# Performance work log

Measured on AMD Instinct MI355X. Metric: run time of the kernel, lower is better.

Reference implementation:

```python
import jax, jax.numpy as jnp
import numpy as np

B, T, C, H = 16, 512, 256, 8
HS_T = C // H   # temporal head size = 32
HS_S = T // H   # spatial head size = 64
EPS = 1e-6


def _ln(x, w, b):
    m = x.mean(-1, keepdims=True)
    v = ((x - m) ** 2).mean(-1, keepdims=True)
    return (x - m) / jnp.sqrt(v + EPS) * w + b


def setup_inputs() -> dict:
    key = jax.random.key(0)
    ks = jax.random.split(key, 16)
    rn = lambda k, s, scale: jax.random.normal(k, s, dtype=jnp.float32) * scale
    inp = {
        "x_T": rn(ks[0], (B, T, C), 1.0),
        "x_S": rn(ks[1], (B, C, T), 1.0),
        # temporal attention: per-head q/k/v projections, stacked [H, hs, C]
        "Wq_t": rn(ks[2], (H, HS_T, C), C ** -0.5),
        "Wk_t": rn(ks[3], (H, HS_T, C), C ** -0.5),
        "Wv_t": rn(ks[4], (H, HS_T, C), C ** -0.5),
        "Wo": rn(ks[5], (C, C), C ** -0.5),
        # spatial attention: per-head q/k over the time axis, stacked [H, hs_s, T]
        "Wq_s": rn(ks[6], (H, HS_S, T), T ** -0.5),
        "Wk_s": rn(ks[7], (H, HS_S, T), T ** -0.5),
        # feed-forward blocks (expansion_factor=4)
        "ff1_w1": rn(ks[8], (4 * C, C), C ** -0.5),
        "ff1_b1": jnp.zeros((4 * C,), jnp.float32),
        "ff1_w2": rn(ks[9], (C, 4 * C), (4 * C) ** -0.5),
        "ff1_b2": jnp.zeros((C,), jnp.float32),
        "ff2_w1": rn(ks[10], (4 * C, C), C ** -0.5),
        "ff2_b1": jnp.zeros((4 * C,), jnp.float32),
        "ff2_w2": rn(ks[11], (C, 4 * C), (4 * C) ** -0.5),
        "ff2_b2": jnp.zeros((C,), jnp.float32),
        # layernorm affine params
        "t_ln1_w": jnp.ones((C,), jnp.float32), "t_ln1_b": jnp.zeros((C,), jnp.float32),
        "t_ln2_w": jnp.ones((C,), jnp.float32), "t_ln2_b": jnp.zeros((C,), jnp.float32),
        "s_ln1_w": jnp.ones((T,), jnp.float32), "s_ln1_b": jnp.zeros((T,), jnp.float32),
        "fus_ln_w": jnp.ones((C,), jnp.float32), "fus_ln_b": jnp.zeros((C,), jnp.float32),
    }
    return inp


def reference(x_T, x_S, Wq_t, Wk_t, Wv_t, Wo, Wq_s, Wk_s,
              ff1_w1, ff1_b1, ff1_w2, ff1_b2, ff2_w1, ff2_b1, ff2_w2, ff2_b2,
              t_ln1_w, t_ln1_b, t_ln2_w, t_ln2_b, s_ln1_w, s_ln1_b,
              fus_ln_w, fus_ln_b):
    # ---- temporal (causal) multi-head attention ----
    h = _ln(x_T, t_ln1_w, t_ln1_b)                         # [B,T,C]
    q = jnp.einsum('btc,hdc->bhtd', h, Wq_t)
    k = jnp.einsum('btc,hdc->bhtd', h, Wk_t)
    v = jnp.einsum('btc,hdc->bhtd', h, Wv_t)
    scores = jnp.einsum('bhtd,bhsd->bhts', q, k) / jnp.sqrt(jnp.float32(HS_T))
    causal = jnp.tril(jnp.ones((T, T), dtype=bool))
    scores = jnp.where(causal, scores, -jnp.inf)
    att = jax.nn.softmax(scores, axis=-1)
    o = jnp.einsum('bhts,bhsd->bhtd', att, v)              # [B,H,T,hs]
    o = o.transpose(0, 2, 1, 3).reshape(B, T, C)           # concat heads
    attn_out = o @ Wo.T
    x = x_T + attn_out
    # FFN 1
    h2 = _ln(x, t_ln2_w, t_ln2_b)
    f = jax.nn.relu(h2 @ ff1_w1.T + ff1_b1) @ ff1_w2.T + ff1_b2
    temporal_out = x + f                                   # [B,T,C]
    # ---- spatial (non-causal) attention over neurons ----
    hs = _ln(x_S, s_ln1_w, s_ln1_b)                        # [B,C,T]
    qs = jnp.einsum('bct,hdt->bhcd', hs, Wq_s)
    ks = jnp.einsum('bct,hdt->bhcd', hs, Wk_s)
    sc = jnp.einsum('bhcd,bhed->bhce', qs, ks) / jnp.sqrt(jnp.float32(HS_S))
    spatial_weights = jax.nn.softmax(sc, axis=-1).mean(axis=1)   # [B,C,C], mean over heads
    # ---- fusion ----
    fused = jnp.einsum('bce,bte->btc', spatial_weights, temporal_out)
    x2 = temporal_out + fused
    h3 = _ln(x2, fus_ln_w, fus_ln_b)
    f2 = jax.nn.relu(h3 @ ff2_w1.T + ff2_b1) @ ff2_w2.T + ff2_b2
    out = x2 + f2
    return out, spatial_weights
```

## Files before the change

kernel.cpp:

```cpp
#include <hip/hip_runtime.h>
#include <hip/hip_bf16.h>

typedef __hip_bfloat16 bf16;
typedef __attribute__((ext_vector_type(8))) short short8;
typedef __attribute__((ext_vector_type(4))) float f32x4;

#define F_BIAS 1
#define F_RELU 2
#define F_RES  4

__device__ __forceinline__ void st_out(float* p, float v){ *p = v; }
__device__ __forceinline__ void st_out(bf16* p, float v){ *p = __float2bfloat16(v); }
__device__ __forceinline__ short f2bs(float f){
  bf16 h = __float2bfloat16(f);
  return *reinterpret_cast<short*>(&h);
}

__device__ __forceinline__ void gl_lds16(const void* g, void* l){
  __builtin_amdgcn_global_load_lds(
      (const __attribute__((address_space(1))) void*)g,
      (__attribute__((address_space(3))) void*)l, 16, 0, 0);
}

struct ProArgs {
  const float* wsrc[10];
  bf16* wdst[10];
  const float *xT, *xS, *tl1w, *tl1b, *sl1w, *sl1b;
  bf16 *hT, *hS;
};

template<int RL>
__device__ __forceinline__ void wave_ln(bf16* __restrict__ dst,
    const float* __restrict__ src, const float* __restrict__ w,
    const float* __restrict__ bvec, int row){
  int lane = threadIdx.x & 63;
  const float* s = src + (size_t)row*RL;
  float4 v0 = *(const float4*)(s + lane*4);
  float4 v1 = {0.f,0.f,0.f,0.f};
  float sum = v0.x+v0.y+v0.z+v0.w;
  float sq  = v0.x*v0.x+v0.y*v0.y+v0.z*v0.z+v0.w*v0.w;
  if (RL == 512){
    v1 = *(const float4*)(s + 256 + lane*4);
    sum += v1.x+v1.y+v1.z+v1.w;
    sq  += v1.x*v1.x+v1.y*v1.y+v1.z*v1.z+v1.w*v1.w;
  }
  #pragma unroll
  for (int off=32; off; off>>=1){
    sum += __shfl_xor(sum, off, 64);
    sq  += __shfl_xor(sq , off, 64);
  }
  const float inv = 1.0f/(float)RL;
  float mean = sum*inv;
  float rstd = rsqrtf(sq*inv - mean*mean + 1e-6f);
  float4 w0 = *(const float4*)(w + lane*4);
  float4 b0 = *(const float4*)(bvec + lane*4);
  bf16* d = dst + (size_t)row*RL;
  short4 o;
  o.x = f2bs((v0.x-mean)*rstd*w0.x + b0.x);
  o.y = f2bs((v0.y-mean)*rstd*w0.y + b0.y);
  o.z = f2bs((v0.z-mean)*rstd*w0.z + b0.z);
  o.w = f2bs((v0.w-mean)*rstd*w0.w + b0.w);
  *(short4*)((short*)d + lane*4) = o;
  if (RL == 512){
    float4 w1 = *(const float4*)(w + 256 + lane*4);
    float4 b1 = *(const float4*)(bvec + 256 + lane*4);
    short4 o1;
    o1.x = f2bs((v1.x-mean)*rstd*w1.x + b1.x);
    o1.y = f2bs((v1.y-mean)*rstd*w1.y + b1.y);
    o1.z = f2bs((v1.z-mean)*rstd*w1.z + b1.z);
    o1.w = f2bs((v1.w-mean)*rstd*w1.w + b1.w);
    *(short4*)((short*)d + 256 + lane*4) = o1;
  }
}

__global__ __launch_bounds__(256) void prologue(ProArgs a){
  int blk = blockIdx.x;
  int wid = threadIdx.x >> 6;
  if (blk < 1792){
    int v = blk*256 + threadIdx.x;
    int e = v*4;
    int seg = (e>=65536)+(e>=131072)+(e>=196608)+(e>=262144)+(e>=524288)
            + (e>=786432)+(e>=1048576)+(e>=1310720)+(e>=1572864);
    const int starts[10] = {0,65536,131072,196608,262144,524288,786432,
                            1048576,1310720,1572864};
    int off = e - starts[seg];
    float4 f = *(const float4*)(a.wsrc[seg] + off);
    short4 o;
    o.x = f2bs(f.x); o.y = f2bs(f.y); o.z = f2bs(f.z); o.w = f2bs(f.w);
    *(short4*)((short*)a.wdst[seg] + off) = o;
  } else if (blk < 1792 + 2048){
    wave_ln<256>(a.hT, a.xT, a.tl1w, a.tl1b, (blk-1792)*4 + wid);
  } else {
    wave_ln<512>(a.hS, a.xS, a.sl1w, a.sl1b, (blk-3840)*4 + wid);
  }
}

template<int BM, int BK>
__device__ __forceinline__ void gemm_body(
    short* __restrict__ AsB, short* __restrict__ BsB,
    const bf16* __restrict__ A, const bf16* __restrict__ B,
    float* __restrict__ outF, bf16* __restrict__ outB,
    const float* __restrict__ bias, const float* __restrict__ resid,
    int K, int lda, int ldb, int ldc, int flags, int m0, int n0){
  int tid = threadIdx.x;
  int w = tid>>6, lane = tid&63, quad = lane>>4, l16 = lane&15;
  constexpr int WM = BM/2;
  constexpr int MF = WM/16;
  constexpr int CPR = BK/8;
  constexpr int CA = BM*CPR/256;
  constexpr int CB = 128*CPR/256;
  int wm = (w>>1)*WM, wn = (w&1)*64;
  f32x4 acc[MF][4];
  #pragma unroll
  for (int r=0;r<MF;r++)
    #pragma unroll
    for (int j=0;j<4;j++)
      acc[r][j] = (f32x4){0.f,0.f,0.f,0.f};

  auto stage = [&](int k0, int half){
    short* as = AsB + half*(BM*BK);
    short* bs = BsB + half*(128*BK);
    #pragma unroll
    for (int c=0;c<CA;c++){
      int ch = tid + c*256;
      int row = ch / CPR, p = ch % CPR;
      gl_lds16(A + (size_t)(m0+row)*lda + k0 + ((p ^ (row&(CPR-1)))*8),
               &as[row*BK + p*8]);
    }
    #pragma unroll
    for (int c=0;c<CB;c++){
      int ch = tid + c*256;
      int row = ch / CPR, p = ch % CPR;
      gl_lds16(B + (size_t)(n0+row)*ldb + k0 + ((p ^ (row&(CPR-1)))*8),
               &bs[row*BK + p*8]);
    }
  };

  stage(0, 0);
  __syncthreads();
  int nk = K / BK;
  for (int t = 0; t < nk; ++t){
    if (t+1 < nk) stage((t+1)*BK, (t+1)&1);
    const short* as = AsB + (t&1)*(BM*BK);
    const short* bs = BsB + (t&1)*(128*BK);
    #pragma unroll
    for (int ks=0; ks<BK/32; ++ks){
      short8 af[MF], bfr[4];
      #pragma unroll
      for (int r=0;r<MF;r++){
        int rr = wm + r*16 + l16;
        af[r] = *(short8*)&as[rr*BK + (((ks*4+quad) ^ (rr&(CPR-1)))*8)];
      }
      #pragma unroll
      for (int j=0;j<4;j++){
        int rr = wn + j*16 + l16;
        bfr[j] = *(short8*)&bs[rr*BK + (((ks*4+quad) ^ (rr&(CPR-1)))*8)];
      }
      #pragma unroll
      for (int r=0;r<MF;r++)
        #pragma unroll
        for (int j=0;j<4;j++)
          acc[r][j] = __builtin_amdgcn_mfma_f32_16x16x32_bf16(af[r], bfr[j], acc[r][j], 0,0,0);
    }
    __syncthreads();
  }
  #pragma unroll
  for (int r=0;r<MF;r++){
    int mb = m0 + wm + r*16 + quad*4;
    #pragma unroll
    for (int j=0;j<4;j++){
      int n = n0 + wn + j*16 + l16;
      float bv = (flags & F_BIAS) ? bias[n] : 0.0f;
      #pragma unroll
      for (int e=0;e<4;e++){
        float v = acc[r][j][e] + bv;
        if (flags & F_RELU) v = fmaxf(v, 0.0f);
        long long idx = (long long)(mb+e)*ldc + n;
        if (flags & F_RES) v += resid[idx];
        if (outF) outF[idx] = v;
        if (outB) st_out(outB + idx, v);
      }
    }
  }
}

template<int BM, int BK>
__global__ __launch_bounds__(256) void gemm_mfma(
    const bf16* __restrict__ A, const bf16* __restrict__ B,
    float* __restrict__ outF, bf16* __restrict__ outB,
    const float* __restrict__ bias, const float* __restrict__ resid,
    int K, int lda, int ldb, int ldc, int flags){
  __shared__ __align__(16) short As[2*BM*BK];
  __shared__ __align__(16) short Bs[2*128*BK];
  gemm_body<BM,BK>(As,Bs,A,B,outF,outB,bias,resid,K,lda,ldb,ldc,flags,
                   blockIdx.x*BM, blockIdx.y*128);
}

struct GArgs {
  const bf16 *A, *B;
  float* outF; bf16* outB;
  const float *bias, *resid;
  int K, lda, ldb, ldc, flags, ty;
};
__global__ __launch_bounds__(256) void gemm_dual(GArgs g0, GArgs g1, int n0){
  __shared__ __align__(16) short As[2*128*64];
  __shared__ __align__(16) short Bs[2*128*64];
  int id = blockIdx.x;
  bool first = id < n0;
  const GArgs& g = first ? g0 : g1;
  int t = first ? id : id - n0;
  int bx = t / g.ty, by = t - bx*g.ty;
  gemm_body<128,64>(As, Bs, g.A, g.B, g.outF, g.outB, g.bias, g.resid,
                    g.K, g.lda, g.ldb, g.ldc, g.flags, bx*128, by*128);
}

__global__ __launch_bounds__(256) void gemm_ln(
    const bf16* __restrict__ A, const bf16* __restrict__ B,
    float* __restrict__ outF, bf16* __restrict__ outLN,
    const float* __restrict__ resid,
    const float* __restrict__ lnw, const float* __restrict__ lnb,
    int K, int lda, int ldb, int flags,
    long long sA, long long sB, long long sO, long long sR){
  int bz = blockIdx.z;
  A += (size_t)bz*sA;
  B += (size_t)bz*sB;
  long long obase = (long long)bz*sO;
  __shared__ __align__(16) short As[2*32*64];
  __shared__ __align__(16) short Bs[2*256*64];
  __shared__ float redS[2][32], redQ[2][32];
  int tid = threadIdx.x;
  int m0 = blockIdx.x*32;
  int w = tid>>6, lane = tid&63, quad = lane>>4, l16 = lane&15;
  int wm = (w>>1)*16, wn = (w&1)*128;
  f32x4 acc[8];
  #pragma unroll
  for (int j=0;j<8;j++) acc[j] = (f32x4){0.f,0.f,0.f,0.f};

  auto stage = [&](int k0, int half){
    short* as = As + half*(32*64);
    short* bs = Bs + half*(256*64);
    {
      int row = tid >> 3, p = tid & 7;
      gl_lds16(A + (size_t)(m0+row)*lda + k0 + ((p ^ (row&7))*8),
               &as[row*64 + p*8]);
    }
    #pragma unroll
    for (int c=0;c<8;c++){
      int ch = tid + c*256;
      int row = ch >> 3, p = ch & 7;
      gl_lds16(B + (size_t)row*ldb + k0 + ((p ^ (row&7))*8),
               &bs[row*64 + p*8]);
    }
  };

  stage(0, 0);
  __syncthreads();
  int nk = K / 64;
  for (int t = 0; t < nk; ++t){
    if (t+1 < nk) stage((t+1)*64, (t+1)&1);
    const short* as = As + (t&1)*(32*64);
    const short* bs = Bs + (t&1)*(256*64);
    #pragma unroll
    for (int ks=0; ks<2; ++ks){
      int rr = wm + l16;
      short8 af = *(short8*)&as[rr*64 + (((ks*4+quad) ^ (rr&7))*8)];
      #pragma unroll
      for (int j=0;j<8;j++){
        int rb = wn + j*16 + l16;
        short8 bfr = *(short8*)&bs[rb*64 + (((ks*4+quad) ^ (rb&7))*8)];
        acc[j] = __builtin_amdgcn_mfma_f32_16x16x32_bf16(af, bfr, acc[j], 0,0,0);
      }
    }
    __syncthreads();
  }
  #pragma unroll
  for (int e=0;e<4;e++){
    int row = wm + quad*4 + e;
    float s = 0.f, q2 = 0.f;
    #pragma unroll
    for (int j=0;j<8;j++){
      float v = acc[j][e];
      if (flags & F_RES)
        v += resid[(long long)bz*sR + (long long)(m0+row)*256 + wn + j*16 + l16];
      acc[j][e] = v;
      s += v; q2 += v*v;
    }
    #pragma unroll
    for (int off=1; off<16; off<<=1){
      s  += __shfl_xor(s , off, 16);
      q2 += __shfl_xor(q2, off, 16);
    }
    if (l16==0){ redS[w&1][row] = s; redQ[w&1][row] = q2; }
  }
  __syncthreads();
  #pragma unroll
  for (int e=0;e<4;e++){
    int row = wm + quad*4 + e;
    float tot = redS[0][row] + redS[1][row];
    float tq  = redQ[0][row] + redQ[1][row];
    float mean = tot * (1.0f/256.0f);
    float var  = tq * (1.0f/256.0f) - mean*mean;
    float rstd = rsqrtf(var + 1e-6f);
    #pragma unroll
    for (int j=0;j<8;j++){
      int col = wn + j*16 + l16;
      float v = acc[j][e];
      long long idx = obase + (long long)(m0+row)*256 + col;
      if (outF) outF[idx] = v;
      outLN[idx] = __float2bfloat16((v-mean)*rstd*lnw[col] + lnb[col]);
    }
  }
}

__device__ __forceinline__ int fsw(int row){ return (row>>1)&3; }
__global__ __launch_bounds__(256) void flash_mfma(
    const bf16* __restrict__ qkv, bf16* __restrict__ o){
  int qt = (int)gridDim.x - 1 - (int)blockIdx.x;
  int h = blockIdx.y, b = blockIdx.z;
  int tid = threadIdx.x;
  int w = tid>>6, lane = tid&63, quad = lane>>4, l16 = lane&15;
  __shared__ __align__(16) bf16 Qs[64*32];
  __shared__ __align__(16) bf16 Ks[2][64*32];
  __shared__ __align__(16) bf16 Vt[2][32*72];
  __shared__ __align__(16) bf16 Ps[64*72];
  const bf16* base = qkv + (size_t)b*512*768;
  int t0 = qt*64;
  int srow = tid>>2, spos = tid&3;
  gl_lds16(base + (size_t)(t0+srow)*768 + h*32 + ((spos ^ fsw(srow))*8),
           &Qs[srow*32 + spos*8]);
  {
    const bf16* rp = base + (size_t)srow*768 + h*32;
    gl_lds16(rp + 256 + ((spos ^ fsw(srow))*8), &Ks[0][srow*32 + spos*8]);
    short8 v = *(const short8*)(rp + 512 + spos*8);
    #pragma unroll
    for (int q=0;q<8;q++){
      short tmp = v[q];
      Vt[0][(spos*8+q)*72 + srow] = *(bf16*)&tmp;
    }
  }
  f32x4 accO[2];
  accO[0] = (f32x4){0.f,0.f,0.f,0.f};
  accO[1] = (f32x4){0.f,0.f,0.f,0.f};
  float m_i[4], l_i[4];
  #pragma unroll
  for (int e=0;e<4;e++){ m_i[e] = -3.0e38f; l_i[e] = 0.0f; }
  const float scale = 0.17677669529663687f;
  __syncthreads();
  int rq = w*16 + l16;
  short8 aq = *(short8*)&Qs[rq*32 + ((quad ^ fsw(rq))*8)];

  for (int kt = 0; kt <= qt; ++kt){
    int cur = kt&1, nxt = cur^1;
    bool pre = (kt < qt);
    short8 vpre;
    if (pre){
      const bf16* rp = base + (size_t)((kt+1)*64 + srow)*768 + h*32;
      gl_lds16(rp + 256 + ((spos ^ fsw(srow))*8), &Ks[nxt][srow*32 + spos*8]);
      vpre = *(const short8*)(rp + 512 + spos*8);
    }
    f32x4 S[4];
    #pragma unroll
    for (int j2=0;j2<4;j2++){
      int rk = j2*16 + l16;
      short8 bk = *(short8*)&Ks[cur][rk*32 + ((quad ^ fsw(rk))*8)];
      S[j2] = __builtin_amdgcn_mfma_f32_16x16x32_bf16(aq, bk,
                (f32x4){0.f,0.f,0.f,0.f}, 0,0,0);
    }
    bool diag = (kt == qt);
    int s0 = kt*64;
    int qrow_base = t0 + w*16 + quad*4;
    #pragma unroll
    for (int e=0;e<4;e++){
      float sv[4];
      #pragma unroll
      for (int j2=0;j2<4;j2++){
        float x = S[j2][e]*scale;
        if (diag && (s0 + j2*16 + l16 > qrow_base + e)) x = -3.0e38f;
        sv[j2] = x;
      }
      float mx = fmaxf(fmaxf(sv[0],sv[1]), fmaxf(sv[2],sv[3]));
      #pragma unroll
      for (int off=1; off<16; off<<=1) mx = fmaxf(mx, __shfl_xor(mx, off, 64));
      float m_new = fmaxf(m_i[e], mx);
      float alpha = __expf(m_i[e]-m_new);
      float rs = 0.0f;
      #pragma unroll
      for (int j2=0;j2<4;j2++){
        float p = __expf(sv[j2]-m_new);
        rs += p;
        Ps[(w*16+quad*4+e)*72 + j2*16 + l16] = __float2bfloat16(p);
      }
      #pragma unroll
      for (int off=1; off<16; off<<=1) rs += __shfl_xor(rs, off, 64);
      l_i[e] = l_i[e]*alpha + rs;
      m_i[e] = m_new;
      accO[0][e] *= alpha;
      accO[1][e] *= alpha;
    }
    asm volatile("s_waitcnt lgkmcnt(0)" ::: "memory");
    __builtin_amdgcn_sched_barrier(0);
    #pragma unroll
    for (int sh=0; sh<2; ++sh){
      short8 ap = *(short8*)&Ps[(w*16+l16)*72 + sh*32 + quad*8];
      #pragma unroll
      for (int dh=0; dh<2; ++dh){
        short8 bv = *(short8*)&Vt[cur][(dh*16+l16)*72 + sh*32 + quad*8];
        accO[dh] = __builtin_amdgcn_mfma_f32_16x16x32_bf16(ap, bv, accO[dh], 0,0,0);
      }
    }
    if (pre){
      #pragma unroll
      for (int q=0;q<8;q++){
        short tmp = vpre[q];
        Vt[nxt][(spos*8+q)*72 + srow] = *(bf16*)&tmp;
      }
    }
    __syncthreads();
  }
  #pragma unroll
  for (int e=0;e<4;e++){
    float inv = 1.0f/l_i[e];
    int t = t0 + w*16 + quad*4 + e;
    bf16* op = o + ((size_t)(b*512+t))*256 + h*32 + l16;
    op[0]  = __float2bfloat16(accO[0][e]*inv);
    op[16] = __float2bfloat16(accO[1][e]*inv);
  }
}

__device__ void spatial_body(bf16* __restrict__ Qall, bf16* __restrict__ KsB,
                             const bf16* __restrict__ qk,
                             float* __restrict__ out1, bf16* __restrict__ swB,
                             int ct, int b){
  int tid = threadIdx.x;
  int w = tid>>6, lane = tid&63, quad = lane>>4, l16 = lane&15;
  __shared__ float redM[4][16], redS2[4][16];
  const bf16* qbase = qk + ((size_t)(b*256 + ct*16))*1024;
  #pragma unroll
  for (int c=0;c<4;c++){
    int ch = tid + c*256;
    int row = ch>>6, p = ch&63;
    gl_lds16(qbase + (size_t)row*1024 + ((p ^ (row&7))*8), &Qall[row*512 + p*8]);
  }
  auto stageK = [&](int h, int half){
    bf16* ks = KsB + half*(256*64);
    #pragma unroll
    for (int c=0;c<8;c++){
      int ch = tid + c*256;
      int e = ch>>3, p = ch&7;
      gl_lds16(qk + ((size_t)(b*256 + e))*1024 + 512 + h*64 + ((p ^ (e&7))*8),
               &ks[e*64 + p*8]);
    }
  };
  stageK(0, 0);
  float fRes[4][4];
  #pragma unroll
  for (int j=0;j<4;j++)
    #pragma unroll
    for (int e=0;e<4;e++) fRes[j][e] = 0.0f;
  __syncthreads();

  for (int h=0; h<8; ++h){
    if (h < 7) stageK(h+1, (h+1)&1);
    const bf16* kcur = KsB + (h&1)*(256*64);
    f32x4 acc[4];
    #pragma unroll
    for (int j=0;j<4;j++) acc[j] = (f32x4){0.f,0.f,0.f,0.f};
    #pragma unroll
    for (int ki=0; ki<2; ++ki){
      int g = h*8 + ki*4 + quad;
      short8 aq = *(short8*)&Qall[l16*512 + ((g ^ (l16&7))*8)];
      #pragma unroll
      for (int j=0;j<4;j++){
        int e = w*64 + j*16 + l16;
        short8 bk = *(short8*)&kcur[e*64 + (((ki*4+quad) ^ (e&7))*8)];
        acc[j] = __builtin_amdgcn_mfma_f32_16x16x32_bf16(aq, bk, acc[j], 0,0,0);
      }
    }
    #pragma unroll
    for (int e=0;e<4;e++){
      float m = -3.0e38f;
      #pragma unroll
      for (int j=0;j<4;j++){
        float s = acc[j][e]*0.125f;
        acc[j][e] = s;
        m = fmaxf(m, s);
      }
      #pragma unroll
      for (int off=1; off<16; off<<=1) m = fmaxf(m, __shfl_xor(m, off, 16));
      if (l16==0) redM[w][quad*4+e] = m;
    }
    __syncthreads();
    #pragma unroll
    for (int e=0;e<4;e++){
      int r = quad*4+e;
      float m = fmaxf(fmaxf(redM[0][r],redM[1][r]), fmaxf(redM[2][r],redM[3][r]));
      float s = 0.0f;
      #pragma unroll
      for (int j=0;j<4;j++){
        float p = __expf(acc[j][e]-m);
        acc[j][e] = p; s += p;
      }
      #pragma unroll
      for (int off=1; off<16; off<<=1) s += __shfl_xor(s, off, 16);
      if (l16==0) redS2[w][r] = s;
    }
    __syncthreads();
    #pragma unroll
    for (int e=0;e<4;e++){
      int r = quad*4+e;
      float tot = redS2[0][r]+redS2[1][r]+redS2[2][r]+redS2[3][r];
      float inv = 0.125f/tot;
      #pragma unroll
      for (int j=0;j<4;j++) fRes[j][e] += acc[j][e]*inv;
    }
  }
  #pragma unroll
  for (int e=0;e<4;e++){
    int c = ct*16 + quad*4 + e;
    size_t rb = ((size_t)b*256 + c)*256;
    #pragma unroll
    for (int j=0;j<4;j++){
      int col = w*64 + j*16 + l16;
      out1[rb+col] = fRes[j][e];
      swB[rb+col]  = __float2bfloat16(fRes[j][e]);
    }
  }
}

__global__ __launch_bounds__(256) void mixed_l2(
    const bf16* __restrict__ gA, const bf16* __restrict__ gB,
    float* __restrict__ gOutF, bf16* __restrict__ gOutB,
    const float* __restrict__ gBias, const float* __restrict__ gResid,
    const bf16* __restrict__ qk, float* __restrict__ out1,
    bf16* __restrict__ swB){
  __shared__ __align__(16) short lds[40960];
  int id = blockIdx.x;
  if (id < 256){
    int bx = id >> 1, by = id & 1;
    gemm_body<64,64>(lds, lds + 2*64*64, gA, gB, gOutF, gOutB, gBias, gResid,
                     1024, 1024, 1024, 256, F_BIAS|F_RES, bx*64, by*128);
  } else {
    int t = id - 256;
    spatial_body((bf16*)lds, (bf16*)(lds + 8192), qk, out1, swB, t & 15, t >> 4);
  }
}

extern "C" void kernel_launch(void* const* d_in, const int* in_sizes, int n_in,
                              void* d_out, int out_size, void* d_ws, size_t ws_size,
                              hipStream_t stream){
  (void)in_sizes; (void)n_in; (void)out_size; (void)ws_size;
  const float* x_T  = (const float*)d_in[0];
  const float* x_S  = (const float*)d_in[1];
  const float* Wq_t = (const float*)d_in[2];
  const float* Wk_t = (const float*)d_in[3];
  const float* Wv_t = (const float*)d_in[4];
  const float* Wo   = (const float*)d_in[5];
  const float* Wq_s = (const float*)d_in[6];
  const float* Wk_s = (const float*)d_in[7];
  const float* f1w1 = (const float*)d_in[8];
  const float* f1b1 = (const float*)d_in[9];
  const float* f1w2 = (const float*)d_in[10];
  const float* f1b2 = (const float*)d_in[11];
  const float* f2w1 = (const float*)d_in[12];
  const float* f2b1 = (const float*)d_in[13];
  const float* f2w2 = (const float*)d_in[14];
  const float* f2b2 = (const float*)d_in[15];
  const float* tl1w = (const float*)d_in[16];
  const float* tl1b = (const float*)d_in[17];
  const float* tl2w = (const float*)d_in[18];
  const float* tl2b = (const float*)d_in[19];
  const float* sl1w = (const float*)d_in[20];
  const float* sl1b = (const float*)d_in[21];
  const float* flw  = (const float*)d_in[22];
  const float* flb  = (const float*)d_in[23];

  float* ws = (float*)d_ws;
  size_t off = 0;
  bf16*  Wqkvb  = (bf16*)(ws + off); off += 768*256/2;
  bf16*  Wob    = (bf16*)(ws + off); off += 256*256/2;
  bf16*  f1w1b  = (bf16*)(ws + off); off += 1024*256/2;
  bf16*  f1w2b  = (bf16*)(ws + off); off += 256*1024/2;
  bf16*  f2w1b  = (bf16*)(ws + off); off += 1024*256/2;
  bf16*  f2w2b  = (bf16*)(ws + off); off += 256*1024/2;
  bf16*  WSb    = (bf16*)(ws + off); off += 1024*512/2;
  bf16*  bufHb  = (bf16*)(ws + off); off += (size_t)8192*256/2;
  bf16*  bufHSb = (bf16*)(ws + off); off += (size_t)4096*512/2;
  bf16*  bufQKVb= (bf16*)(ws + off); off += (size_t)8192*768/2;
  bf16*  bufBigB= (bf16*)(ws + off); off += (size_t)8192*1024/2;
  bf16*  bufOb  = (bf16*)(ws + off); off += (size_t)8192*256/2;
  bf16*  bufTOb = (bf16*)(ws + off); off += (size_t)8192*256/2;
  bf16*  swB    = (bf16*)(ws + off); off += (size_t)16*256*256/2;
  bf16*  qkB    = (bf16*)(ws + off); off += (size_t)4096*1024/2;
  float* bufX   = ws + off; off += (size_t)8192*256;
  float* bufTO  = ws + off; off += (size_t)8192*256;
  float* bufX2  = ws + off; off += (size_t)8192*256;

  float* out0 = (float*)d_out;
  float* out1 = out0 + (size_t)16*512*256;

  ProArgs pa;
  pa.wsrc[0]=Wq_t;  pa.wdst[0]=Wqkvb;
  pa.wsrc[1]=Wk_t;  pa.wdst[1]=Wqkvb+65536;
  pa.wsrc[2]=Wv_t;  pa.wdst[2]=Wqkvb+131072;
  pa.wsrc[3]=Wo;    pa.wdst[3]=Wob;
  pa.wsrc[4]=f1w1;  pa.wdst[4]=f1w1b;
  pa.wsrc[5]=f1w2;  pa.wdst[5]=f1w2b;
  pa.wsrc[6]=f2w1;  pa.wdst[6]=f2w1b;
  pa.wsrc[7]=f2w2;  pa.wdst[7]=f2w2b;
  pa.wsrc[8]=Wq_s;  pa.wdst[8]=WSb;
  pa.wsrc[9]=Wk_s;  pa.wdst[9]=WSb+262144;
  pa.xT=x_T; pa.xS=x_S; pa.tl1w=tl1w; pa.tl1b=tl1b;
  pa.sl1w=sl1w; pa.sl1b=sl1b; pa.hT=bufHb; pa.hS=bufHSb;
  prologue<<<4864,256,0,stream>>>(pa);

  GArgs gq, gs;
  gq.A=bufHb;  gq.B=Wqkvb; gq.outF=nullptr; gq.outB=bufQKVb;
  gq.bias=nullptr; gq.resid=nullptr;
  gq.K=256; gq.lda=256; gq.ldb=256; gq.ldc=768; gq.flags=0; gq.ty=6;
  gs.A=bufHSb; gs.B=WSb;   gs.outF=nullptr; gs.outB=qkB;
  gs.bias=nullptr; gs.resid=nullptr;
  gs.K=512; gs.lda=512; gs.ldb=512; gs.ldc=1024; gs.flags=0; gs.ty=8;
  gemm_dual<<<640,256,0,stream>>>(gq, gs, 384);

  flash_mfma<<<dim3(8,8,16),256,0,stream>>>(bufQKVb, bufOb);
  gemm_ln<<<dim3(256,1,1),256,0,stream>>>(bufOb, Wob, bufX, bufHb,
        x_T, tl2w, tl2b, 256, 256,256, F_RES, 0,0,0,0);
  gemm_mfma<128,64><<<dim3(64,8),256,0,stream>>>(bufHb, f1w1b, nullptr, bufBigB,
        f1b1, nullptr, 256, 256,256,1024, F_BIAS|F_RELU);
  mixed_l2<<<512,256,0,stream>>>(bufBigB, f1w2b, bufTO, bufTOb, f1b2, bufX,
        qkB, out1, swB);
  gemm_ln<<<dim3(16,1,16),256,0,stream>>>(bufTOb, swB, bufX2, bufHb,
        bufTO, flw, flb, 256, 256,256, F_RES,
        131072, 65536, 131072, 131072);
  gemm_mfma<128,64><<<dim3(64,8),256,0,stream>>>(bufHb, f2w1b, nullptr, bufBigB,
        f2b1, nullptr, 256, 256,256,1024, F_BIAS|F_RELU);
  gemm_mfma<64,64><<<dim3(128,2),256,0,stream>>>(bufBigB, f2w2b, out0, nullptr,
        f2b2, bufX2, 1024, 1024,1024,256, F_BIAS|F_RES);
}
```

Before: 303.4 us.

## Shrink GEMM tiles, widen gemm_ln to 512 threads, split spatial K staging

Generalizes gemm_body to separate BM/BN tiles and halves M tiles for the QKV, FFN and second-layer GEMMs, doubling block counts to fill more CUs. gemm_ln now runs with 8 waves, each covering 64 columns. The spatial attention body stages K in half-head chunks to cut LDS use, which lets mixed_l2 use a smaller shared buffer. The loop barriers move to the top of each iteration, dropping one sync per pipeline step, and LDS-only barriers use an lgkmcnt wait. Smaller tiles give more parallelism but less reuse per block and more redundant loads of B.

```diff
diff --git a/kernel.cpp b/kernel.cpp
--- a/kernel.cpp
+++ b/kernel.cpp
@@ -20,6 +20,11 @@
   __builtin_amdgcn_global_load_lds(
       (const __attribute__((address_space(1))) void*)g,
       (__attribute__((address_space(3))) void*)l, 16, 0, 0);
+}
+
+__device__ __forceinline__ void lgkm_barrier(){
+  asm volatile("s_waitcnt lgkmcnt(0)" ::: "memory");
+  __builtin_amdgcn_s_barrier();
 }
 
 struct ProArgs {
@@ -95,7 +100,7 @@
   }
 }
 
-template<int BM, int BK>
+template<int BM, int BN, int BK>
 __device__ __forceinline__ void gemm_body(
     short* __restrict__ AsB, short* __restrict__ BsB,
     const bf16* __restrict__ A, const bf16* __restrict__ B,
@@ -104,22 +109,22 @@
     int K, int lda, int ldb, int ldc, int flags, int m0, int n0){
   int tid = threadIdx.x;
   int w = tid>>6, lane = tid&63, quad = lane>>4, l16 = lane&15;
-  constexpr int WM = BM/2;
-  constexpr int MF = WM/16;
+  constexpr int MF  = BM/32;
+  constexpr int NF  = BN/32;
   constexpr int CPR = BK/8;
-  constexpr int CA = BM*CPR/256;
-  constexpr int CB = 128*CPR/256;
-  int wm = (w>>1)*WM, wn = (w&1)*64;
-  f32x4 acc[MF][4];
+  constexpr int CA  = BM*CPR/256;
+  constexpr int CB  = BN*CPR/256;
+  int wm = (w>>1)*(BM/2), wn = (w&1)*(BN/2);
+  f32x4 acc[MF][NF];
   #pragma unroll
   for (int r=0;r<MF;r++)
     #pragma unroll
-    for (int j=0;j<4;j++)
+    for (int j=0;j<NF;j++)
       acc[r][j] = (f32x4){0.f,0.f,0.f,0.f};
 
   auto stage = [&](int k0, int half){
     short* as = AsB + half*(BM*BK);
-    short* bs = BsB + half*(128*BK);
+    short* bs = BsB + half*(BN*BK);
     #pragma unroll
     for (int c=0;c<CA;c++){
       int ch = tid + c*256;
@@ -137,38 +142,37 @@
   };
 
   stage(0, 0);
-  __syncthreads();
   int nk = K / BK;
   for (int t = 0; t < nk; ++t){
+    __syncthreads();
     if (t+1 < nk) stage((t+1)*BK, (t+1)&1);
     const short* as = AsB + (t&1)*(BM*BK);
-    const short* bs = BsB + (t&1)*(128*BK);
+    const short* bs = BsB + (t&1)*(BN*BK);
     #pragma unroll
     for (int ks=0; ks<BK/32; ++ks){
-      short8 af[MF], bfr[4];
+      short8 af[MF], bfr[NF];
       #pragma unroll
       for (int r=0;r<MF;r++){
         int rr = wm + r*16 + l16;
         af[r] = *(short8*)&as[rr*BK + (((ks*4+quad) ^ (rr&(CPR-1)))*8)];
       }
       #pragma unroll
-      for (int j=0;j<4;j++){
+      for (int j=0;j<NF;j++){
         int rr = wn + j*16 + l16;
         bfr[j] = *(short8*)&bs[rr*BK + (((ks*4+quad) ^ (rr&(CPR-1)))*8)];
       }
       #pragma unroll
       for (int r=0;r<MF;r++)
         #pragma unroll
-        for (int j=0;j<4;j++)
+        for (int j=0;j<NF;j++)
           acc[r][j] = __builtin_amdgcn_mfma_f32_16x16x32_bf16(af[r], bfr[j], acc[r][j], 0,0,0);
     }
-    __syncthreads();
   }
   #pragma unroll
   for (int r=0;r<MF;r++){
     int mb = m0 + wm + r*16 + quad*4;
     #pragma unroll
-    for (int j=0;j<4;j++){
+    for (int j=0;j<NF;j++){
       int n = n0 + wn + j*16 + l16;
       float bv = (flags & F_BIAS) ? bias[n] : 0.0f;
       #pragma unroll
@@ -184,16 +188,16 @@
   }
 }
 
-template<int BM, int BK>
+template<int BM, int BN, int BK>
 __global__ __launch_bounds__(256) void gemm_mfma(
     const bf16* __restrict__ A, const bf16* __restrict__ B,
     float* __restrict__ outF, bf16* __restrict__ outB,
     const float* __restrict__ bias, const float* __restrict__ resid,
     int K, int lda, int ldb, int ldc, int flags){
   __shared__ __align__(16) short As[2*BM*BK];
-  __shared__ __align__(16) short Bs[2*128*BK];
-  gemm_body<BM,BK>(As,Bs,A,B,outF,outB,bias,resid,K,lda,ldb,ldc,flags,
-                   blockIdx.x*BM, blockIdx.y*128);
+  __shared__ __align__(16) short Bs[2*BN*BK];
+  gemm_body<BM,BN,BK>(As,Bs,A,B,outF,outB,bias,resid,K,lda,ldb,ldc,flags,
+                      blockIdx.x*BM, blockIdx.y*BN);
 }
 
 struct GArgs {
@@ -203,18 +207,18 @@
   int K, lda, ldb, ldc, flags, ty;
 };
 __global__ __launch_bounds__(256) void gemm_dual(GArgs g0, GArgs g1, int n0){
-  __shared__ __align__(16) short As[2*128*64];
+  __shared__ __align__(16) short As[2*64*64];
   __shared__ __align__(16) short Bs[2*128*64];
   int id = blockIdx.x;
   bool first = id < n0;
   const GArgs& g = first ? g0 : g1;
   int t = first ? id : id - n0;
   int bx = t / g.ty, by = t - bx*g.ty;
-  gemm_body<128,64>(As, Bs, g.A, g.B, g.outF, g.outB, g.bias, g.resid,
-                    g.K, g.lda, g.ldb, g.ldc, g.flags, bx*128, by*128);
-}
-
-__global__ __launch_bounds__(256) void gemm_ln(
+  gemm_body<64,128,64>(As, Bs, g.A, g.B, g.outF, g.outB, g.bias, g.resid,
+                       g.K, g.lda, g.ldb, g.ldc, g.flags, bx*64, by*128);
+}
+
+__global__ __launch_bounds__(512) void gemm_ln(
     const bf16* __restrict__ A, const bf16* __restrict__ B,
     float* __restrict__ outF, bf16* __restrict__ outLN,
     const float* __restrict__ resid,
@@ -227,26 +231,27 @@
   long long obase = (long long)bz*sO;
   __shared__ __align__(16) short As[2*32*64];
   __shared__ __align__(16) short Bs[2*256*64];
-  __shared__ float redS[2][32], redQ[2][32];
+  __shared__ float redS[4][32], redQ[4][32];
   int tid = threadIdx.x;
   int m0 = blockIdx.x*32;
   int w = tid>>6, lane = tid&63, quad = lane>>4, l16 = lane&15;
-  int wm = (w>>1)*16, wn = (w&1)*128;
-  f32x4 acc[8];
-  #pragma unroll
-  for (int j=0;j<8;j++) acc[j] = (f32x4){0.f,0.f,0.f,0.f};
+  int wm = (w>>2)*16;
+  int wn = (w&3)*64;
+  f32x4 acc[4];
+  #pragma unroll
+  for (int j=0;j<4;j++) acc[j] = (f32x4){0.f,0.f,0.f,0.f};
 
   auto stage = [&](int k0, int half){
     short* as = As + half*(32*64);
     short* bs = Bs + half*(256*64);
-    {
+    if (tid < 256){
       int row = tid >> 3, p = tid & 7;
       gl_lds16(A + (size_t)(m0+row)*lda + k0 + ((p ^ (row&7))*8),
                &as[row*64 + p*8]);
     }
     #pragma unroll
-    for (int c=0;c<8;c++){
-      int ch = tid + c*256;
+    for (int c=0;c<4;c++){
+      int ch = tid + c*512;
       int row = ch >> 3, p = ch & 7;
       gl_lds16(B + (size_t)row*ldb + k0 + ((p ^ (row&7))*8),
                &bs[row*64 + p*8]);
@@ -254,9 +259,9 @@
   };
 
   stage(0, 0);
-  __syncthreads();
   int nk = K / 64;
   for (int t = 0; t < nk; ++t){
+    __syncthreads();
     if (t+1 < nk) stage((t+1)*64, (t+1)&1);
     const short* as = As + (t&1)*(32*64);
     const short* bs = Bs + (t&1)*(256*64);
@@ -265,20 +270,19 @@
       int rr = wm + l16;
       short8 af = *(short8*)&as[rr*64 + (((ks*4+quad) ^ (rr&7))*8)];
       #pragma unroll
-      for (int j=0;j<8;j++){
+      for (int j=0;j<4;j++){
         int rb = wn + j*16 + l16;
         short8 bfr = *(short8*)&bs[rb*64 + (((ks*4+quad) ^ (rb&7))*8)];
         acc[j] = __builtin_amdgcn_mfma_f32_16x16x32_bf16(af, bfr, acc[j], 0,0,0);
       }
     }
-    __syncthreads();
   }
   #pragma unroll
   for (int e=0;e<4;e++){
     int row = wm + quad*4 + e;
     float s = 0.f, q2 = 0.f;
     #pragma unroll
-    for (int j=0;j<8;j++){
+    for (int j=0;j<4;j++){
       float v = acc[j][e];
       if (flags & F_RES)
         v += resid[(long long)bz*sR + (long long)(m0+row)*256 + wn + j*16 + l16];
@@ -290,19 +294,19 @@
       s  += __shfl_xor(s , off, 16);
       q2 += __shfl_xor(q2, off, 16);
     }
-    if (l16==0){ redS[w&1][row] = s; redQ[w&1][row] = q2; }
+    if (l16==0){ redS[w&3][row] = s; redQ[w&3][row] = q2; }
   }
   __syncthreads();
   #pragma unroll
   for (int e=0;e<4;e++){
     int row = wm + quad*4 + e;
-    float tot = redS[0][row] + redS[1][row];
-    float tq  = redQ[0][row] + redQ[1][row];
+    float tot = redS[0][row] + redS[1][row] + redS[2][row] + redS[3][row];
+    float tq  = redQ[0][row] + redQ[1][row] + redQ[2][row] + redQ[3][row];
     float mean = tot * (1.0f/256.0f);
     float var  = tq * (1.0f/256.0f) - mean*mean;
     float rstd = rsqrtf(var + 1e-6f);
     #pragma unroll
-    for (int j=0;j<8;j++){
+    for (int j=0;j<4;j++){
       int col = wn + j*16 + l16;
       float v = acc[j][e];
       long long idx = obase + (long long)(m0+row)*256 + col;
@@ -350,6 +354,7 @@
   short8 aq = *(short8*)&Qs[rq*32 + ((quad ^ fsw(rq))*8)];
 
   for (int kt = 0; kt <= qt; ++kt){
+    if (kt) __syncthreads();
     int cur = kt&1, nxt = cur^1;
     bool pre = (kt < qt);
     short8 vpre;
@@ -415,7 +420,6 @@
         Vt[nxt][(spos*8+q)*72 + srow] = *(bf16*)&tmp;
       }
     }
-    __syncthreads();
   }
   #pragma unroll
   for (int e=0;e<4;e++){
@@ -441,77 +445,84 @@
     int row = ch>>6, p = ch&63;
     gl_lds16(qbase + (size_t)row*1024 + ((p ^ (row&7))*8), &Qall[row*512 + p*8]);
   }
-  auto stageK = [&](int h, int half){
-    bf16* ks = KsB + half*(256*64);
-    #pragma unroll
-    for (int c=0;c<8;c++){
+  auto stageK = [&](int ck, int half){
+    bf16* ks = KsB + half*(128*64);
+    int h = ck>>1, hf = ck&1;
+    #pragma unroll
+    for (int c=0;c<4;c++){
       int ch = tid + c*256;
-      int e = ch>>3, p = ch&7;
-      gl_lds16(qk + ((size_t)(b*256 + e))*1024 + 512 + h*64 + ((p ^ (e&7))*8),
-               &ks[e*64 + p*8]);
+      int el = ch>>3, p = ch&7;
+      int e  = hf*128 + el;
+      gl_lds16(qk + ((size_t)(b*256 + e))*1024 + 512 + h*64 + ((p ^ (el&7))*8),
+               &ks[el*64 + p*8]);
     }
   };
   stageK(0, 0);
   float fRes[4][4];
   #pragma unroll
-  for (int j=0;j<4;j++)
-    #pragma unroll
-    for (int e=0;e<4;e++) fRes[j][e] = 0.0f;
-  __syncthreads();
-
-  for (int h=0; h<8; ++h){
-    if (h < 7) stageK(h+1, (h+1)&1);
-    const bf16* kcur = KsB + (h&1)*(256*64);
-    f32x4 acc[4];
-    #pragma unroll
-    for (int j=0;j<4;j++) acc[j] = (f32x4){0.f,0.f,0.f,0.f};
+  for (int f=0;f<4;f++)
+    #pragma unroll
+    for (int e=0;e<4;e++) fRes[f][e] = 0.0f;
+  f32x4 acc[4];
+
+  for (int ck=0; ck<16; ++ck){
+    int h = ck>>1, hf = ck&1;
+    __syncthreads();
+    if (ck+1 < 16) stageK(ck+1, (ck+1)&1);
+    const bf16* kcur = KsB + (ck&1)*(128*64);
+    if (hf == 0){
+      #pragma unroll
+      for (int f=0;f<4;f++) acc[f] = (f32x4){0.f,0.f,0.f,0.f};
+    }
     #pragma unroll
     for (int ki=0; ki<2; ++ki){
       int g = h*8 + ki*4 + quad;
       short8 aq = *(short8*)&Qall[l16*512 + ((g ^ (l16&7))*8)];
       #pragma unroll
-      for (int j=0;j<4;j++){
-        int e = w*64 + j*16 + l16;
-        short8 bk = *(short8*)&kcur[e*64 + (((ki*4+quad) ^ (e&7))*8)];
-        acc[j] = __builtin_amdgcn_mfma_f32_16x16x32_bf16(aq, bk, acc[j], 0,0,0);
-      }
-    }
-    #pragma unroll
-    for (int e=0;e<4;e++){
-      float m = -3.0e38f;
-      #pragma unroll
-      for (int j=0;j<4;j++){
-        float s = acc[j][e]*0.125f;
-        acc[j][e] = s;
-        m = fmaxf(m, s);
-      }
-      #pragma unroll
-      for (int off=1; off<16; off<<=1) m = fmaxf(m, __shfl_xor(m, off, 16));
-      if (l16==0) redM[w][quad*4+e] = m;
-    }
-    __syncthreads();
-    #pragma unroll
-    for (int e=0;e<4;e++){
-      int r = quad*4+e;
-      float m = fmaxf(fmaxf(redM[0][r],redM[1][r]), fmaxf(redM[2][r],redM[3][r]));
-      float s = 0.0f;
-      #pragma unroll
-      for (int j=0;j<4;j++){
-        float p = __expf(acc[j][e]-m);
-        acc[j][e] = p; s += p;
-      }
-      #pragma unroll
-      for (int off=1; off<16; off<<=1) s += __shfl_xor(s, off, 16);
-      if (l16==0) redS2[w][r] = s;
-    }
-    __syncthreads();
-    #pragma unroll
-    for (int e=0;e<4;e++){
-      int r = quad*4+e;
-      float tot = redS2[0][r]+redS2[1][r]+redS2[2][r]+redS2[3][r];
-      float inv = 0.125f/tot;
-      #pragma unroll
-      for (int j=0;j<4;j++) fRes[j][e] += acc[j][e]*inv;
+      for (int j=0;j<2;j++){
+        int el = w*32 + j*16 + l16;
+        short8 bk = *(short8*)&kcur[el*64 + (((ki*4+quad) ^ (el&7))*8)];
+        acc[hf*2+j] = __builtin_amdgcn_mfma_f32_16x16x32_bf16(aq, bk, acc[hf*2+j], 0,0,0);
+      }
+    }
+    if (hf == 1){
+      #pragma unroll
+      for (int e=0;e<4;e++){
+        float m = -3.0e38f;
+        #pragma unroll
+        for (int f=0;f<4;f++){
+          float s = acc[f][e]*0.125f;
+          acc[f][e] = s;
+          m = fmaxf(m, s);
+        }
+        #pragma unroll
+        for (int off=1; off<16; off<<=1) m = fmaxf(m, __shfl_xor(m, off, 16));
+        if (l16==0) redM[w][quad*4+e] = m;
+      }
+      lgkm_barrier();
+      #pragma unroll
+      for (int e=0;e<4;e++){
+        int r = quad*4+e;
+        float m = fmaxf(fmaxf(redM[0][r],redM[1][r]), fmaxf(redM[2][r],redM[3][r]));
+        float s = 0.0f;
+        #pragma unroll
+        for (int f=0;f<4;f++){
+          float p = __expf(acc[f][e]-m);
+          acc[f][e] = p; s += p;
+        }
+        #pragma unroll
+        for (int off=1; off<16; off<<=1) s += __shfl_xor(s, off, 16);
+        if (l16==0) redS2[w][r] = s;
+      }
+      lgkm_barrier();
+      #pragma unroll
+      for (int e=0;e<4;e++){
+        int r = quad*4+e;
+        float tot = redS2[0][r]+redS2[1][r]+redS2[2][r]+redS2[3][r];
+        float inv = 0.125f/tot;
+        #pragma unroll
+        for (int f=0;f<4;f++) fRes[f][e] += acc[f][e]*inv;
+      }
     }
   }
   #pragma unroll
@@ -519,10 +530,10 @@
     int c = ct*16 + quad*4 + e;
     size_t rb = ((size_t)b*256 + c)*256;
     #pragma unroll
-    for (int j=0;j<4;j++){
-      int col = w*64 + j*16 + l16;
-      out1[rb+col] = fRes[j][e];
-      swB[rb+col]  = __float2bfloat16(fRes[j][e]);
+    for (int f=0;f<4;f++){
+      int col = (f>>1)*128 + w*32 + (f&1)*16 + l16;
+      out1[rb+col] = fRes[f][e];
+      swB[rb+col]  = __float2bfloat16(fRes[f][e]);
     }
   }
 }
@@ -533,14 +544,14 @@
     const float* __restrict__ gBias, const float* __restrict__ gResid,
     const bf16* __restrict__ qk, float* __restrict__ out1,
     bf16* __restrict__ swB){
-  __shared__ __align__(16) short lds[40960];
+  __shared__ __align__(16) short lds[24576];
   int id = blockIdx.x;
-  if (id < 256){
+  if (id < 512){
     int bx = id >> 1, by = id & 1;
-    gemm_body<64,64>(lds, lds + 2*64*64, gA, gB, gOutF, gOutB, gBias, gResid,
-                     1024, 1024, 1024, 256, F_BIAS|F_RES, bx*64, by*128);
+    gemm_body<32,128,64>(lds, lds + 2*32*64, gA, gB, gOutF, gOutB, gBias, gResid,
+                         1024, 1024, 1024, 256, F_BIAS|F_RES, bx*32, by*128);
   } else {
-    int t = id - 256;
+    int t = id - 512;
     spatial_body((bf16*)lds, (bf16*)(lds + 8192), qk, out1, swB, t & 15, t >> 4);
   }
 }
@@ -620,20 +631,20 @@
   gs.A=bufHSb; gs.B=WSb;   gs.outF=nullptr; gs.outB=qkB;
   gs.bias=nullptr; gs.resid=nullptr;
   gs.K=512; gs.lda=512; gs.ldb=512; gs.ldc=1024; gs.flags=0; gs.ty=8;
-  gemm_dual<<<640,256,0,stream>>>(gq, gs, 384);
+  gemm_dual<<<1280,256,0,stream>>>(gq, gs, 768);
 
   flash_mfma<<<dim3(8,8,16),256,0,stream>>>(bufQKVb, bufOb);
-  gemm_ln<<<dim3(256,1,1),256,0,stream>>>(bufOb, Wob, bufX, bufHb,
+  gemm_ln<<<dim3(256,1,1),512,0,stream>>>(bufOb, Wob, bufX, bufHb,
         x_T, tl2w, tl2b, 256, 256,256, F_RES, 0,0,0,0);
-  gemm_mfma<128,64><<<dim3(64,8),256,0,stream>>>(bufHb, f1w1b, nullptr, bufBigB,
+  gemm_mfma<64,128,64><<<dim3(128,8),256,0,stream>>>(bufHb, f1w1b, nullptr, bufBigB,
         f1b1, nullptr, 256, 256,256,1024, F_BIAS|F_RELU);
-  mixed_l2<<<512,256,0,stream>>>(bufBigB, f1w2b, bufTO, bufTOb, f1b2, bufX,
+  mixed_l2<<<768,256,0,stream>>>(bufBigB, f1w2b, bufTO, bufTOb, f1b2, bufX,
         qkB, out1, swB);
-  gemm_ln<<<dim3(16,1,16),256,0,stream>>>(bufTOb, swB, bufX2, bufHb,
+  gemm_ln<<<dim3(16,1,16),512,0,stream>>>(bufTOb, swB, bufX2, bufHb,
         bufTO, flw, flb, 256, 256,256, F_RES,
         131072, 65536, 131072, 131072);
-  gemm_mfma<128,64><<<dim3(64,8),256,0,stream>>>(bufHb, f2w1b, nullptr, bufBigB,
+  gemm_mfma<64,128,64><<<dim3(128,8),256,0,stream>>>(bufHb, f2w1b, nullptr, bufBigB,
         f2b1, nullptr, 256, 256,256,1024, F_BIAS|F_RELU);
-  gemm_mfma<64,64><<<dim3(128,2),256,0,stream>>>(bufBigB, f2w2b, out0, nullptr,
+  gemm_mfma<32,128,64><<<dim3(256,2),256,0,stream>>>(bufBigB, f2w2b, out0, nullptr,
         f2b2, bufX2, 1024, 1024,1024,256, F_BIAS|F_RES);
 }
```

After: 300.9 us. Within noise of the previous version (-0.8%).
